# Optimization experiments

Measured on AMD Instinct MI355X. Metric: run time of the kernel, lower is better.

Reference implementation:

```python
import jax, jax.numpy as jnp
import numpy as np

D_MODEL = 1024
NUM_HEADS = 16
HEAD_DIM = D_MODEL // NUM_HEADS


def setup_inputs() -> dict:
    key = jax.random.key(0)
    ks = jax.random.split(key, 11)
    B, N = 2, 2048
    s = 1.0 / np.sqrt(D_MODEL)
    return {
        "query": jax.random.normal(ks[0], (B, N, D_MODEL), jnp.float32),
        "key":   jax.random.normal(ks[1], (B, N, D_MODEL), jnp.float32),
        "value": jax.random.normal(ks[2], (B, N, D_MODEL), jnp.float32),
        "Wq": jax.random.normal(ks[3], (D_MODEL, D_MODEL), jnp.float32) * s,
        "bq": jax.random.normal(ks[4], (D_MODEL,), jnp.float32) * 0.01,
        "Wk": jax.random.normal(ks[5], (D_MODEL, D_MODEL), jnp.float32) * s,
        "bk": jax.random.normal(ks[6], (D_MODEL,), jnp.float32) * 0.01,
        "Wv": jax.random.normal(ks[7], (D_MODEL, D_MODEL), jnp.float32) * s,
        "bv": jax.random.normal(ks[8], (D_MODEL,), jnp.float32) * 0.01,
        "Wo": jax.random.normal(ks[9], (D_MODEL, D_MODEL), jnp.float32) * s,
        "bo": jax.random.normal(ks[10], (D_MODEL,), jnp.float32) * 0.01,
    }


def _split_heads(x):
    # [B, N, d_model] -> [B, H, N, head_dim]
    B, N, _ = x.shape
    return x.reshape(B, N, NUM_HEADS, HEAD_DIM).transpose(0, 2, 1, 3)


def reference(query, key, value, Wq, bq, Wk, bk, Wv, bv, Wo, bo):
    B, N, _ = query.shape
    q = _split_heads(query @ Wq.T + bq)  # [B,H,N,dh]
    k = _split_heads(key @ Wk.T + bk)
    v = _split_heads(value @ Wv.T + bv)
    # NOTE: faithful to source: no 1/sqrt(head_dim) scaling.
    scores = jnp.einsum("bhnd,bhmd->bhnm", q, k)
    attn = jax.nn.softmax(scores, axis=-1)
    out = jnp.einsum("bhnm,bhmd->bhnd", attn, v)
    out = out.transpose(0, 2, 1, 3).reshape(B, N, D_MODEL)
    return out @ Wo.T + bo
```

## Files before the change

kernel.cpp:

```cpp
#include <hip/hip_runtime.h>
#include <cstdint>

#define DEV __device__ __forceinline__

typedef __bf16 bf16x8 __attribute__((ext_vector_type(8)));
typedef __bf16 bf16x4v __attribute__((ext_vector_type(4)));
typedef short s16x4 __attribute__((ext_vector_type(4)));
typedef short s16x8 __attribute__((ext_vector_type(8)));
typedef float f32x4 __attribute__((ext_vector_type(4)));
typedef unsigned short u16;

constexpr int D_MODEL = 1024;
constexpr int SEQ = 2048;
constexpr float LOG2E = 1.4426950408889634f;
constexpr float SHIFT = 64.0f;

DEV u16 f2bf(float f) {
  uint32_t u = __float_as_uint(f);
  u += 0x7fff + ((u >> 16) & 1);
  return (u16)(u >> 16);
}

DEV void load_lds16(const void* g, void* l) {
  __builtin_amdgcn_global_load_lds((const __attribute__((address_space(1))) void*)g,
                                   (__attribute__((address_space(3))) void*)l, 16, 0, 0);
}

DEV f32x4 mfma16_bf16(s16x4 a, s16x4 b, f32x4 c) {
#if __has_builtin(__builtin_amdgcn_mfma_f32_16x16x16bf16_1k)
  return __builtin_amdgcn_mfma_f32_16x16x16bf16_1k(a, b, c, 0, 0, 0);
#else
  f32x4 d;
  asm("v_mfma_f32_16x16x16_bf16 %0, %1, %2, %3" : "=v"(d) : "v"(a), "v"(b), "v"(c));
  return d;
#endif
}

struct ConvArgs {
  const float* src[7];
  u16* dst[7];
  int n[7];
};

__global__ __launch_bounds__(256) void convert_kernel(ConvArgs a) {
  const int t = blockIdx.y;
  const int i = (blockIdx.x * 256 + threadIdx.x) * 4;
  if (i >= a.n[t]) return;
  const float4 v = *(const float4*)(a.src[t] + i);
  ushort4 o;
  o.x = f2bf(v.x); o.y = f2bf(v.y); o.z = f2bf(v.z); o.w = f2bf(v.w);
  *(ushort4*)(a.dst[t] + i) = o;
}

struct GemmArgs {
  const u16* A[3];
  const u16* W[3];
  const float* bias[3];
  void* out[3];
  float scale[3];
  int mode;
};

__global__ __launch_bounds__(256) void gemm_nt(GemmArgs args) {
  __shared__ u16 lA[128 * 64];
  __shared__ u16 lB[128 * 64];
  const int z = blockIdx.z;
  const u16* __restrict__ A = args.A[z];
  const u16* __restrict__ W = args.W[z];
  const int tid = threadIdx.x;
  const int lane = tid & 63, wid = tid >> 6;
  const int quad = lane >> 4, l16 = lane & 15;
  const int wm = wid >> 1, wn = wid & 1;
  const int m0 = blockIdx.y * 128;
  const int n0 = blockIdx.x * 128;

  f32x4 acc[4][4] = {};

  for (int kt = 0; kt < D_MODEL / 64; ++kt) {
    const int k0 = kt * 64;
#pragma unroll
    for (int p = 0; p < 4; ++p) {
      int c = p * 256 + tid;
      int row = c >> 3;
      int g = ((c & 7) ^ (row & 7)) * 8;
      load_lds16(A + (size_t)(m0 + row) * D_MODEL + k0 + g, &lA[c * 8]);
      load_lds16(W + (size_t)(n0 + row) * D_MODEL + k0 + g, &lB[c * 8]);
    }
    __syncthreads();
#pragma unroll
    for (int ks = 0; ks < 2; ++ks) {
      bf16x8 af[4], bfr[4];
#pragma unroll
      for (int mt = 0; mt < 4; ++mt) {
        int r = wm * 64 + mt * 16 + l16;
        int ch = (ks * 4 + quad) ^ (r & 7);
        af[mt] = *(const bf16x8*)&lA[r * 64 + ch * 8];
      }
#pragma unroll
      for (int nt = 0; nt < 4; ++nt) {
        int r = wn * 64 + nt * 16 + l16;
        int ch = (ks * 4 + quad) ^ (r & 7);
        bfr[nt] = *(const bf16x8*)&lB[r * 64 + ch * 8];
      }
#pragma unroll
      for (int mt = 0; mt < 4; ++mt)
#pragma unroll
        for (int nt = 0; nt < 4; ++nt)
          acc[mt][nt] = __builtin_amdgcn_mfma_f32_16x16x32_bf16(af[mt], bfr[nt], acc[mt][nt], 0, 0, 0);
    }
    __syncthreads();
  }

  const float* __restrict__ bias = args.bias[z];
  if (args.mode == 0) {
    u16* out = (u16*)args.out[z];
    float sc = args.scale[z];
#pragma unroll
    for (int nt = 0; nt < 4; ++nt) {
      int col = n0 + wn * 64 + nt * 16 + l16;
      float bv = bias[col];
      int h = col >> 6, d = col & 63;
#pragma unroll
      for (int mt = 0; mt < 4; ++mt) {
        int mb = m0 + wm * 64 + mt * 16 + quad * 4;
#pragma unroll
        for (int r = 0; r < 4; ++r) {
          int tok = mb + r;
          int b = tok >> 11, tt = tok & 2047;
          out[(((size_t)(b * 16 + h) * SEQ + tt) << 6) + d] = f2bf((acc[mt][nt][r] + bv) * sc);
        }
      }
    }
  } else {
    float* out = (float*)args.out[z];
#pragma unroll
    for (int nt = 0; nt < 4; ++nt) {
      int col = n0 + wn * 64 + nt * 16 + l16;
      float bv = bias[col];
#pragma unroll
      for (int mt = 0; mt < 4; ++mt) {
        int mb = m0 + wm * 64 + mt * 16 + quad * 4;
#pragma unroll
        for (int r = 0; r < 4; ++r)
          out[(size_t)(mb + r) * D_MODEL + col] = acc[mt][nt][r] + bv;
      }
    }
  }
}

__global__ __launch_bounds__(256) void transpose_v(const u16* __restrict__ V, u16* __restrict__ Vt) {
  __shared__ u16 tile[64][66];
  const int bh = blockIdx.y;
  const int t0 = blockIdx.x * 64;
  const int tid = threadIdx.x;
  const u16* src = V + ((size_t)bh * SEQ + t0) * 64;
#pragma unroll
  for (int p = 0; p < 4; ++p) {
    int v = p * 256 + tid;
    int row = v >> 4, c4 = (v & 15) * 4;
    ushort4 x = *(const ushort4*)(src + (size_t)row * 64 + c4);
    tile[row][c4] = x.x; tile[row][c4 + 1] = x.y; tile[row][c4 + 2] = x.z; tile[row][c4 + 3] = x.w;
  }
  __syncthreads();
  u16* dst = Vt + (size_t)bh * 64 * SEQ + t0;
#pragma unroll
  for (int p = 0; p < 4; ++p) {
    int v = p * 256 + tid;
    int d = v >> 4, c4 = (v & 15) * 4;
    ushort4 o;
    o.x = tile[c4][d]; o.y = tile[c4 + 1][d]; o.z = tile[c4 + 2][d]; o.w = tile[c4 + 3][d];
    *(ushort4*)(dst + (size_t)d * SEQ + c4) = o;
  }
}

__global__ __launch_bounds__(128) void attn_kernel(const u16* __restrict__ Q,
                                                   const u16* __restrict__ K,
                                                   const u16* __restrict__ Vt,
                                                   u16* __restrict__ O) {
  __shared__ u16 lK[64 * 64];
  __shared__ u16 lV[80 * 64];
  const int bid = blockIdx.x;
  const int xcd = bid & 7, jj = bid >> 3;
  const int bh = xcd + 8 * (jj >> 5);
  const int q0 = (jj & 31) * 64;
  const int tid = threadIdx.x;
  const int lane = tid & 63, w = tid >> 6;
  const int quad = lane >> 4, l16 = lane & 15;

  const u16* kbase = K + (size_t)bh * SEQ * 64;
  const u16* vtbase = Vt + (size_t)bh * 64 * SEQ;

  {
    int idx = tid * 8;
    int row = 64 + (idx >> 6);
    int addr = row * 64 + ((((idx & 63) >> 3) ^ (row & 7)) * 8);
    u16 val = (row == 64) ? (u16)0x3F80 : (u16)0;
    ushort4 o = {val, val, val, val};
    *(ushort4*)&lV[addr] = o;
    *(ushort4*)&lV[addr + 4] = o;
  }

  bf16x8 qf[2][2];
#pragma unroll
  for (int qh = 0; qh < 2; ++qh) {
    const u16* qrow = Q + ((size_t)bh * SEQ + q0 + w * 32 + qh * 16 + l16) * 64;
    qf[qh][0] = *(const bf16x8*)(qrow + quad * 8);
    qf[qh][1] = *(const bf16x8*)(qrow + 32 + quad * 8);
  }

  f32x4 acc[2][5] = {};
  const f32x4 minit = {-SHIFT, -SHIFT, -SHIFT, -SHIFT};

  for (int t = 0; t < SEQ / 64; ++t) {
    __syncthreads();
#pragma unroll
    for (int p = 0; p < 4; ++p) {
      int c = p * 128 + tid;
      int row = c >> 3;
      int kperm = (row & 3) | (((row >> 2) & 3) << 4) | (((row >> 4) & 3) << 2);
      int g = ((c & 7) ^ (row & 7)) * 8;
      load_lds16(kbase + (size_t)(t * 64 + kperm) * 64 + g, &lK[c * 8]);
      load_lds16(vtbase + (size_t)row * SEQ + t * 64 + g, &lV[c * 8]);
    }
    __syncthreads();

    s16x4 pf[2][4];
#pragma unroll
    for (int nt = 0; nt < 4; ++nt) {
      int r = nt * 16 + l16;
      bf16x8 k0 = *(const bf16x8*)&lK[r * 64 + ((quad ^ (r & 7)) * 8)];
      bf16x8 k1 = *(const bf16x8*)&lK[r * 64 + (((4 + quad) ^ (r & 7)) * 8)];
#pragma unroll
      for (int qh = 0; qh < 2; ++qh) {
        f32x4 a0 = __builtin_amdgcn_mfma_f32_16x16x32_bf16(k0, qf[qh][0], minit, 0, 0, 0);
        f32x4 sv = __builtin_amdgcn_mfma_f32_16x16x32_bf16(k1, qf[qh][1], a0, 0, 0, 0);
        bf16x4v pb;
#pragma unroll
        for (int r2 = 0; r2 < 4; ++r2)
          pb[r2] = (__bf16)__builtin_amdgcn_exp2f(sv[r2]);
        pf[qh][nt] = __builtin_bit_cast(s16x4, pb);
      }
    }

#pragma unroll
    for (int dt = 0; dt < 5; ++dt) {
      int row = dt * 16 + l16;
      bf16x8 v0 = *(const bf16x8*)&lV[row * 64 + (((2 * quad) ^ (row & 7)) * 8)];
      bf16x8 v1 = *(const bf16x8*)&lV[row * 64 + (((2 * quad + 1) ^ (row & 7)) * 8)];
      s16x8 v0s = __builtin_bit_cast(s16x8, v0);
      s16x8 v1s = __builtin_bit_cast(s16x8, v1);
      s16x4 vf[4];
      vf[0] = __builtin_shufflevector(v0s, v0s, 0, 1, 2, 3);
      vf[1] = __builtin_shufflevector(v0s, v0s, 4, 5, 6, 7);
      vf[2] = __builtin_shufflevector(v1s, v1s, 0, 1, 2, 3);
      vf[3] = __builtin_shufflevector(v1s, v1s, 4, 5, 6, 7);
#pragma unroll
      for (int qh = 0; qh < 2; ++qh)
#pragma unroll
        for (int kt = 0; kt < 4; ++kt)
          acc[qh][dt] = mfma16_bf16(vf[kt], pf[qh][kt], acc[qh][dt]);
    }
  }

  const int b = bh >> 4, h = bh & 15;
#pragma unroll
  for (int qh = 0; qh < 2; ++qh) {
    float sum = __shfl(acc[qh][4][0], l16, 64);
    float inv = 1.0f / sum;
    const int tok = b * SEQ + q0 + w * 32 + qh * 16 + l16;
    u16* obase = O + (size_t)tok * D_MODEL + h * 64;
#pragma unroll
    for (int dt = 0; dt < 4; ++dt) {
      ushort4 o;
      o.x = f2bf(acc[qh][dt][0] * inv);
      o.y = f2bf(acc[qh][dt][1] * inv);
      o.z = f2bf(acc[qh][dt][2] * inv);
      o.w = f2bf(acc[qh][dt][3] * inv);
      *(ushort4*)(obase + dt * 16 + quad * 4) = o;
    }
  }
}

extern "C" void kernel_launch(void* const* d_in, const int* in_sizes, int n_in,
                              void* d_out, int out_size, void* d_ws, size_t ws_size,
                              hipStream_t stream) {
  const float* q  = (const float*)d_in[0];
  const float* k  = (const float*)d_in[1];
  const float* v  = (const float*)d_in[2];
  const float* Wq = (const float*)d_in[3];
  const float* bq = (const float*)d_in[4];
  const float* Wk = (const float*)d_in[5];
  const float* bk = (const float*)d_in[6];
  const float* Wv = (const float*)d_in[7];
  const float* bv = (const float*)d_in[8];
  const float* Wo = (const float*)d_in[9];
  const float* bo = (const float*)d_in[10];

  uint8_t* ws = (uint8_t*)d_ws;
  const size_t MB = 1024 * 1024;
  u16* Xq  = (u16*)(ws + 0 * MB);
  u16* Xk  = (u16*)(ws + 8 * MB);
  u16* Xv  = (u16*)(ws + 16 * MB);
  u16* Wqb = (u16*)(ws + 24 * MB);
  u16* Wkb = (u16*)(ws + 26 * MB);
  u16* Wvb = (u16*)(ws + 28 * MB);
  u16* Wob = (u16*)(ws + 30 * MB);
  u16* Qb  = (u16*)(ws + 32 * MB);
  u16* Kb  = (u16*)(ws + 40 * MB);
  u16* Vb  = (u16*)(ws + 48 * MB);
  u16* Vtb = Xk;
  u16* Ob  = Xq;

  ConvArgs ca;
  ca.src[0] = q;  ca.dst[0] = Xq;  ca.n[0] = 4194304;
  ca.src[1] = k;  ca.dst[1] = Xk;  ca.n[1] = 4194304;
  ca.src[2] = v;  ca.dst[2] = Xv;  ca.n[2] = 4194304;
  ca.src[3] = Wq; ca.dst[3] = Wqb; ca.n[3] = 1048576;
  ca.src[4] = Wk; ca.dst[4] = Wkb; ca.n[4] = 1048576;
  ca.src[5] = Wv; ca.dst[5] = Wvb; ca.n[5] = 1048576;
  ca.src[6] = Wo; ca.dst[6] = Wob; ca.n[6] = 1048576;
  convert_kernel<<<dim3(4096, 7), 256, 0, stream>>>(ca);

  GemmArgs ga;
  ga.A[0] = Xq; ga.A[1] = Xk; ga.A[2] = Xv;
  ga.W[0] = Wqb; ga.W[1] = Wkb; ga.W[2] = Wvb;
  ga.bias[0] = bq; ga.bias[1] = bk; ga.bias[2] = bv;
  ga.out[0] = Qb; ga.out[1] = Kb; ga.out[2] = Vb;
  ga.scale[0] = LOG2E; ga.scale[1] = 1.0f; ga.scale[2] = 1.0f;
  ga.mode = 0;
  gemm_nt<<<dim3(8, 32, 3), 256, 0, stream>>>(ga);

  transpose_v<<<dim3(32, 32), 256, 0, stream>>>(Vb, Vtb);

  attn_kernel<<<dim3(1024), 128, 0, stream>>>(Qb, Kb, Vtb, Ob);

  GemmArgs g2;
  g2.A[0] = Ob; g2.A[1] = Ob; g2.A[2] = Ob;
  g2.W[0] = Wob; g2.W[1] = Wob; g2.W[2] = Wob;
  g2.bias[0] = bo; g2.bias[1] = bo; g2.bias[2] = bo;
  g2.out[0] = d_out; g2.out[1] = d_out; g2.out[2] = d_out;
  g2.scale[0] = 1.0f; g2.scale[1] = 1.0f; g2.scale[2] = 1.0f;
  g2.mode = 1;
  gemm_nt<<<dim3(8, 32, 1), 256, 0, stream>>>(g2);
}
```

Before: 246.1 us.

## Double-buffer K/V tiles and split keys across waves in attention kernel

Restructures the attention kernel so each wave processes all 64 queries against half of the 64-key tile, with a cross-wave reduction of accumulators through shared memory at the end. K/V tiles are double-buffered, prefetching the next tile while computing the current one, which removes one barrier per iteration. The PV product now uses 16x16x32 MFMAs instead of 16x16x16, and the row-sum comes from a ones-vector MFMA instead of a padded V row. The cost is more accumulator registers (4x5 f32x4) and doubled LDS, bounded by launch_bounds(128,2).

```diff
diff --git a/kernel.cpp b/kernel.cpp
--- a/kernel.cpp
+++ b/kernel.cpp
@@ -4,8 +4,6 @@
 #define DEV __device__ __forceinline__
 
 typedef __bf16 bf16x8 __attribute__((ext_vector_type(8)));
-typedef __bf16 bf16x4v __attribute__((ext_vector_type(4)));
-typedef short s16x4 __attribute__((ext_vector_type(4)));
 typedef short s16x8 __attribute__((ext_vector_type(8)));
 typedef float f32x4 __attribute__((ext_vector_type(4)));
 typedef unsigned short u16;
@@ -24,16 +22,6 @@
 DEV void load_lds16(const void* g, void* l) {
   __builtin_amdgcn_global_load_lds((const __attribute__((address_space(1))) void*)g,
                                    (__attribute__((address_space(3))) void*)l, 16, 0, 0);
-}
-
-DEV f32x4 mfma16_bf16(s16x4 a, s16x4 b, f32x4 c) {
-#if __has_builtin(__builtin_amdgcn_mfma_f32_16x16x16bf16_1k)
-  return __builtin_amdgcn_mfma_f32_16x16x16bf16_1k(a, b, c, 0, 0, 0);
-#else
-  f32x4 d;
-  asm("v_mfma_f32_16x16x16_bf16 %0, %1, %2, %3" : "=v"(d) : "v"(a), "v"(b), "v"(c));
-  return d;
-#endif
 }
 
 struct ConvArgs {
@@ -173,12 +161,11 @@
   }
 }
 
-__global__ __launch_bounds__(128) void attn_kernel(const u16* __restrict__ Q,
-                                                   const u16* __restrict__ K,
-                                                   const u16* __restrict__ Vt,
-                                                   u16* __restrict__ O) {
-  __shared__ u16 lK[64 * 64];
-  __shared__ u16 lV[80 * 64];
+__global__ __launch_bounds__(128, 2) void attn_kernel(const u16* __restrict__ Q,
+                                                      const u16* __restrict__ K,
+                                                      const u16* __restrict__ Vt,
+                                                      u16* __restrict__ O) {
+  __shared__ u16 sm[2][2][64 * 64];
   const int bid = blockIdx.x;
   const int xcd = bid & 7, jj = bid >> 3;
   const int bh = xcd + 8 * (jj >> 5);
@@ -190,93 +177,121 @@
   const u16* kbase = K + (size_t)bh * SEQ * 64;
   const u16* vtbase = Vt + (size_t)bh * 64 * SEQ;
 
-  {
-    int idx = tid * 8;
-    int row = 64 + (idx >> 6);
-    int addr = row * 64 + ((((idx & 63) >> 3) ^ (row & 7)) * 8);
-    u16 val = (row == 64) ? (u16)0x3F80 : (u16)0;
-    ushort4 o = {val, val, val, val};
-    *(ushort4*)&lV[addr] = o;
-    *(ushort4*)&lV[addr + 4] = o;
-  }
-
-  bf16x8 qf[2][2];
-#pragma unroll
-  for (int qh = 0; qh < 2; ++qh) {
-    const u16* qrow = Q + ((size_t)bh * SEQ + q0 + w * 32 + qh * 16 + l16) * 64;
+  bf16x8 qf[4][2];
+#pragma unroll
+  for (int qh = 0; qh < 4; ++qh) {
+    const u16* qrow = Q + ((size_t)bh * SEQ + q0 + qh * 16 + l16) * 64;
     qf[qh][0] = *(const bf16x8*)(qrow + quad * 8);
     qf[qh][1] = *(const bf16x8*)(qrow + 32 + quad * 8);
   }
 
-  f32x4 acc[2][5] = {};
+  bf16x8 onesA;
+  {
+    __bf16 v = (l16 == 0) ? (__bf16)1.0f : (__bf16)0.0f;
+#pragma unroll
+    for (int j = 0; j < 8; ++j) onesA[j] = v;
+  }
+
+  f32x4 acc[4][5] = {};
   const f32x4 minit = {-SHIFT, -SHIFT, -SHIFT, -SHIFT};
 
+#define STAGE(T, B)                                                               \
+  {                                                                               \
+    _Pragma("unroll")                                                             \
+    for (int p = 0; p < 4; ++p) {                                                 \
+      int c = p * 128 + tid;                                                      \
+      int row = c >> 3;                                                           \
+      int km = (row & 32) | (((row >> 2) & 3) << 3) | (((row >> 4) & 1) << 2) |   \
+               (row & 3);                                                         \
+      int g = ((c & 7) ^ (row & 7)) * 8;                                          \
+      load_lds16(kbase + (size_t)((T) * 64 + km) * 64 + g, &sm[B][0][c * 8]);     \
+      load_lds16(vtbase + (size_t)row * SEQ + (T) * 64 + g, &sm[B][1][c * 8]);    \
+    }                                                                             \
+  }
+
+  STAGE(0, 0);
+  __syncthreads();
+
   for (int t = 0; t < SEQ / 64; ++t) {
+    if (t + 1 < SEQ / 64) STAGE(t + 1, (t + 1) & 1);
+    const u16* lK = sm[t & 1][0];
+    const u16* lV = sm[t & 1][1];
+
+    bf16x8 kf[2][2];
+#pragma unroll
+    for (int nt = 0; nt < 2; ++nt) {
+      int r = w * 32 + nt * 16 + l16;
+#pragma unroll
+      for (int ks = 0; ks < 2; ++ks) {
+        int ch = (ks * 4 + quad) ^ (r & 7);
+        kf[nt][ks] = *(const bf16x8*)&lK[r * 64 + ch * 8];
+      }
+    }
+
+    s16x8 pf[4];
+#pragma unroll
+    for (int qh = 0; qh < 4; ++qh) {
+      f32x4 s0 = __builtin_amdgcn_mfma_f32_16x16x32_bf16(kf[0][0], qf[qh][0], minit, 0, 0, 0);
+      s0 = __builtin_amdgcn_mfma_f32_16x16x32_bf16(kf[0][1], qf[qh][1], s0, 0, 0, 0);
+      f32x4 s1 = __builtin_amdgcn_mfma_f32_16x16x32_bf16(kf[1][0], qf[qh][0], minit, 0, 0, 0);
+      s1 = __builtin_amdgcn_mfma_f32_16x16x32_bf16(kf[1][1], qf[qh][1], s1, 0, 0, 0);
+      bf16x8 pb;
+#pragma unroll
+      for (int r = 0; r < 4; ++r) {
+        pb[r] = (__bf16)__builtin_amdgcn_exp2f(s0[r]);
+        pb[4 + r] = (__bf16)__builtin_amdgcn_exp2f(s1[r]);
+      }
+      pf[qh] = __builtin_bit_cast(s16x8, pb);
+    }
+
+#pragma unroll
+    for (int dt = 0; dt < 4; ++dt) {
+      int row = dt * 16 + l16;
+      int ch = (w * 4 + quad) ^ (row & 7);
+      bf16x8 vf = *(const bf16x8*)&lV[row * 64 + ch * 8];
+#pragma unroll
+      for (int qh = 0; qh < 4; ++qh)
+        acc[qh][dt] = __builtin_amdgcn_mfma_f32_16x16x32_bf16(
+            vf, __builtin_bit_cast(bf16x8, pf[qh]), acc[qh][dt], 0, 0, 0);
+    }
+#pragma unroll
+    for (int qh = 0; qh < 4; ++qh)
+      acc[qh][4] = __builtin_amdgcn_mfma_f32_16x16x32_bf16(
+          onesA, __builtin_bit_cast(bf16x8, pf[qh]), acc[qh][4], 0, 0, 0);
+
     __syncthreads();
-#pragma unroll
-    for (int p = 0; p < 4; ++p) {
-      int c = p * 128 + tid;
-      int row = c >> 3;
-      int kperm = (row & 3) | (((row >> 2) & 3) << 4) | (((row >> 4) & 3) << 2);
-      int g = ((c & 7) ^ (row & 7)) * 8;
-      load_lds16(kbase + (size_t)(t * 64 + kperm) * 64 + g, &lK[c * 8]);
-      load_lds16(vtbase + (size_t)row * SEQ + t * 64 + g, &lV[c * 8]);
-    }
-    __syncthreads();
-
-    s16x4 pf[2][4];
-#pragma unroll
-    for (int nt = 0; nt < 4; ++nt) {
-      int r = nt * 16 + l16;
-      bf16x8 k0 = *(const bf16x8*)&lK[r * 64 + ((quad ^ (r & 7)) * 8)];
-      bf16x8 k1 = *(const bf16x8*)&lK[r * 64 + (((4 + quad) ^ (r & 7)) * 8)];
-#pragma unroll
-      for (int qh = 0; qh < 2; ++qh) {
-        f32x4 a0 = __builtin_amdgcn_mfma_f32_16x16x32_bf16(k0, qf[qh][0], minit, 0, 0, 0);
-        f32x4 sv = __builtin_amdgcn_mfma_f32_16x16x32_bf16(k1, qf[qh][1], a0, 0, 0, 0);
-        bf16x4v pb;
-#pragma unroll
-        for (int r2 = 0; r2 < 4; ++r2)
-          pb[r2] = (__bf16)__builtin_amdgcn_exp2f(sv[r2]);
-        pf[qh][nt] = __builtin_bit_cast(s16x4, pb);
-      }
-    }
-
-#pragma unroll
-    for (int dt = 0; dt < 5; ++dt) {
-      int row = dt * 16 + l16;
-      bf16x8 v0 = *(const bf16x8*)&lV[row * 64 + (((2 * quad) ^ (row & 7)) * 8)];
-      bf16x8 v1 = *(const bf16x8*)&lV[row * 64 + (((2 * quad + 1) ^ (row & 7)) * 8)];
-      s16x8 v0s = __builtin_bit_cast(s16x8, v0);
-      s16x8 v1s = __builtin_bit_cast(s16x8, v1);
-      s16x4 vf[4];
-      vf[0] = __builtin_shufflevector(v0s, v0s, 0, 1, 2, 3);
-      vf[1] = __builtin_shufflevector(v0s, v0s, 4, 5, 6, 7);
-      vf[2] = __builtin_shufflevector(v1s, v1s, 0, 1, 2, 3);
-      vf[3] = __builtin_shufflevector(v1s, v1s, 4, 5, 6, 7);
-#pragma unroll
-      for (int qh = 0; qh < 2; ++qh)
-#pragma unroll
-        for (int kt = 0; kt < 4; ++kt)
-          acc[qh][dt] = mfma16_bf16(vf[kt], pf[qh][kt], acc[qh][dt]);
-    }
-  }
-
-  const int b = bh >> 4, h = bh & 15;
-#pragma unroll
-  for (int qh = 0; qh < 2; ++qh) {
-    float sum = __shfl(acc[qh][4][0], l16, 64);
-    float inv = 1.0f / sum;
-    const int tok = b * SEQ + q0 + w * 32 + qh * 16 + l16;
-    u16* obase = O + (size_t)tok * D_MODEL + h * 64;
-#pragma unroll
-    for (int dt = 0; dt < 4; ++dt) {
-      ushort4 o;
-      o.x = f2bf(acc[qh][dt][0] * inv);
-      o.y = f2bf(acc[qh][dt][1] * inv);
-      o.z = f2bf(acc[qh][dt][2] * inv);
-      o.w = f2bf(acc[qh][dt][3] * inv);
-      *(ushort4*)(obase + dt * 16 + quad * 4) = o;
+  }
+#undef STAGE
+
+  float* red = (float*)&sm[0][0][0];
+  if (w == 1) {
+#pragma unroll
+    for (int qh = 0; qh < 4; ++qh)
+#pragma unroll
+      for (int dt = 0; dt < 5; ++dt)
+        *(f32x4*)&red[((qh * 5 + dt) * 64 + lane) * 4] = acc[qh][dt];
+  }
+  __syncthreads();
+  if (w == 0) {
+    const int b = bh >> 4, h = bh & 15;
+#pragma unroll
+    for (int qh = 0; qh < 4; ++qh) {
+#pragma unroll
+      for (int dt = 0; dt < 5; ++dt)
+        acc[qh][dt] += *(const f32x4*)&red[((qh * 5 + dt) * 64 + lane) * 4];
+      float sum = __shfl(acc[qh][4][0], l16, 64);
+      float inv = 1.0f / sum;
+      const int tok = b * SEQ + q0 + qh * 16 + l16;
+      u16* obase = O + (size_t)tok * D_MODEL + h * 64;
+#pragma unroll
+      for (int dt = 0; dt < 4; ++dt) {
+        ushort4 o;
+        o.x = f2bf(acc[qh][dt][0] * inv);
+        o.y = f2bf(acc[qh][dt][1] * inv);
+        o.z = f2bf(acc[qh][dt][2] * inv);
+        o.w = f2bf(acc[qh][dt][3] * inv);
+        *(ushort4*)(obase + dt * 16 + quad * 4) = o;
+      }
     }
   }
 }
```

New measurement: 231.2 us. 1.06x faster.
